# Performance work log

Hardware: AMD Instinct MI355X
Metric: run time of the kernel (lower is better)

The kernel has to match this reference:

```python
import jax, jax.numpy as jnp
import numpy as np

V, E, H, O, T = 50000, 300, 512, 64, 21
B, S = 256, 128


def setup_inputs() -> dict:
    key = jax.random.key(0)
    ks = jax.random.split(key, 20)
    u = lambda k, shape, s: jax.random.uniform(k, shape, jnp.float32, -s, s)
    sg = 1.0 / np.sqrt(H)
    s2 = 1.0 / np.sqrt(2 * H)
    return {
        "x": jax.random.randint(ks[0], (B, S), 0, V),
        "ner_tags": jax.random.randint(ks[1], (B, S), 0, T),
        "mask": jnp.ones((B, S), dtype=bool),
        "emb": jax.random.normal(ks[2], (V, E), jnp.float32) * 0.1,
        "W_ih_f": u(ks[3], (3 * H, E), sg),
        "W_hh_f": u(ks[4], (3 * H, H), sg),
        "b_ih_f": u(ks[5], (3 * H,), sg),
        "b_hh_f": u(ks[6], (3 * H,), sg),
        "W_ih_b": u(ks[7], (3 * H, E), sg),
        "W_hh_b": u(ks[8], (3 * H, H), sg),
        "b_ih_b": u(ks[9], (3 * H,), sg),
        "b_hh_b": u(ks[10], (3 * H,), sg),
        "attn_w": u(ks[11], (1, 2 * H), s2),
        "attn_b": u(ks[12], (1,), s2),
        "fc_w": u(ks[13], (O, 2 * H), s2),
        "fc_b": u(ks[14], (O,), s2),
        "ner_w": u(ks[15], (T, 2 * H), s2),
        "ner_b": u(ks[16], (T,), s2),
        "crf_start": u(ks[17], (T,), 0.1),
        "crf_end": u(ks[18], (T,), 0.1),
        "crf_trans": u(ks[19], (T, T), 0.1),
    }


def _gru_dir(xp, h0, W_hh, b_hh, reverse):
    # xp: [S, B, 3H] precomputed input projections (PyTorch GRU gate order r,z,n)
    def step(h, xpt):
        hp = h @ W_hh.T + b_hh
        xr, xz, xn = jnp.split(xpt, 3, axis=-1)
        hr, hz, hn = jnp.split(hp, 3, axis=-1)
        r = jax.nn.sigmoid(xr + hr)
        z = jax.nn.sigmoid(xz + hz)
        n = jnp.tanh(xn + r * hn)
        h_new = (1.0 - z) * n + z * h
        return h_new, h_new
    _, hs = jax.lax.scan(step, h0, xp, reverse=reverse)
    return hs  # [S, B, H]


def _crf_nll(emissions, tags, mask, start, end, trans):
    # emissions: [B, S, T]; torchcrf forward algorithm, reduction='mean'
    dt = emissions.dtype
    em_t = jnp.transpose(emissions, (1, 0, 2))        # [S, B, T]
    m_t = jnp.transpose(mask, (1, 0))                  # [S, B]

    def step(score, inp):
        em, m = inp
        # [B,T,1] + [1,T,T] + [B,1,T] -> logsumexp over prev tag
        ns = jax.nn.logsumexp(score[:, :, None] + trans[None] + em[:, None, :], axis=1)
        score = jnp.where(m[:, None], ns, score)
        return score, None

    score0 = start[None, :] + em_t[0]
    score, _ = jax.lax.scan(step, score0, (em_t[1:], m_t[1:]))
    logZ = jax.nn.logsumexp(score + end[None, :], axis=1)  # [B]

    mf = mask.astype(dt)
    em_sc = jnp.take_along_axis(emissions, tags[..., None], axis=2)[..., 0]  # [B,S]
    tr_sc = trans[tags[:, :-1], tags[:, 1:]]                                  # [B,S-1]
    seq_ends = jnp.sum(mask, axis=1).astype(jnp.int32) - 1
    last_tags = jnp.take_along_axis(tags, seq_ends[:, None].astype(tags.dtype), axis=1)[:, 0]
    num = (start[tags[:, 0]] + em_sc[:, 0]
           + jnp.sum((em_sc[:, 1:] + tr_sc) * mf[:, 1:], axis=1)
           + end[last_tags])
    return -jnp.mean(num - logZ)


def _forward(x, ner_tags, mask, emb,
             W_ih_f, W_hh_f, b_ih_f, b_hh_f,
             W_ih_b, W_hh_b, b_ih_b, b_hh_b,
             attn_w, attn_b, fc_w, fc_b, ner_w, ner_b,
             crf_start, crf_end, crf_trans):
    b = x.shape[0]
    xe = emb[x]                                  # [B,S,E]
    xs = jnp.transpose(xe, (1, 0, 2))            # [S,B,E]
    h0 = jnp.zeros((b, H), dtype=emb.dtype)
    xpf = jnp.einsum('sbe,ge->sbg', xs, W_ih_f) + b_ih_f
    hf = _gru_dir(xpf, h0, W_hh_f, b_hh_f, False)
    xpb = jnp.einsum('sbe,ge->sbg', xs, W_ih_b) + b_ih_b
    hb = _gru_dir(xpb, h0, W_hh_b, b_hh_b, True)
    gru_out = jnp.transpose(jnp.concatenate([hf, hb], axis=-1), (1, 0, 2))  # [B,S,2H]

    # attention pooling over seq dim (no masking, as in original)
    scores = gru_out @ attn_w.T + attn_b          # [B,S,1]
    w = jax.nn.softmax(scores, axis=1)
    ctx = jnp.sum(w * gru_out, axis=1)            # [B,2H]
    intent_logits = ctx @ fc_w.T + fc_b           # [B,O]  (dropout = identity in eval)

    emissions = gru_out @ ner_w.T + ner_b         # [B,S,T]
    ner_loss = _crf_nll(emissions, ner_tags, mask, crf_start, crf_end, crf_trans)
    return intent_logits, ner_loss


def reference(x, ner_tags, mask, emb,
              W_ih_f, W_hh_f, b_ih_f, b_hh_f,
              W_ih_b, W_hh_b, b_ih_b, b_hh_b,
              attn_w, attn_b, fc_w, fc_b, ner_w, ner_b,
              crf_start, crf_end, crf_trans):
    return _forward(x, ner_tags, mask, emb,
                    W_ih_f, W_hh_f, b_ih_f, b_hh_f,
                    W_ih_b, W_hh_b, b_ih_b, b_hh_b,
                    attn_w, attn_b, fc_w, fc_b, ner_w, ner_b,
                    crf_start, crf_end, crf_trans)
```

## Files before the change

### kernel.cpp

```cpp
#include <hip/hip_runtime.h>
#include <hip/hip_cooperative_groups.h>
#include <stdint.h>

namespace cg = cooperative_groups;

typedef __attribute__((ext_vector_type(8))) short s8_t;
typedef __attribute__((ext_vector_type(4))) short s4v_t;
typedef __attribute__((ext_vector_type(4))) float f4_t;
typedef unsigned short u16;

#define V_  50000
#define E_  300
#define EP_ 320
#define H_  512
#define G_  1536
#define O_  64
#define T_  21
#define B_  256
#define S_  128
#define BS_ 32768

__device__ __forceinline__ float b2f(u16 u) {
    union { unsigned int u; float f; } v; v.u = ((unsigned int)u) << 16; return v.f;
}
__device__ __forceinline__ u16 f2b(float f) {
    union { float f; unsigned int u; } v; v.f = f;
    unsigned int r = v.u + 0x7fffu + ((v.u >> 16) & 1u);
    return (u16)(r >> 16);
}
__device__ __forceinline__ float fsig(float x) {
    return __builtin_amdgcn_rcpf(1.f + __expf(-x));
}
__device__ __forceinline__ float ftanh(float x) {
    return 1.f - 2.f * __builtin_amdgcn_rcpf(1.f + __expf(2.f * x));
}

__global__ void prep_kernel(const float* wih_f, const float* wih_b,
                            const float* whh_f, const float* whh_b,
                            const float* ner_w,
                            u16* wih_bf, u16* whh_bf, u16* nerw_bf)
{
    const int NW = 3072 * EP_;
    const int NH = 2 * G_ * H_;
    const int NN = 32 * 1024;
    int stride = gridDim.x * blockDim.x;
    for (int i = blockIdx.x * blockDim.x + threadIdx.x; i < NW + NH + NN; i += stride) {
        if (i < NW) {
            int n = i / EP_, k = i % EP_;
            float v = 0.f;
            if (k < E_) v = (n < G_) ? wih_f[n * E_ + k] : wih_b[(n - G_) * E_ + k];
            wih_bf[i] = f2b(v);
        } else if (i < NW + NH) {
            int j = i - NW;
            int d = j / (G_ * H_), r = j % (G_ * H_);
            whh_bf[j] = f2b(d == 0 ? whh_f[r] : whh_b[r]);
        } else {
            int j = i - NW - NH;
            int t = j / 1024, k = j % 1024;
            nerw_bf[j] = f2b(t < T_ ? ner_w[t * 1024 + k] : 0.f);
        }
    }
}

__global__ void gather_kernel(const int* x, const float* emb, u16* xe)
{
    int stride = gridDim.x * blockDim.x;
    for (int i = blockIdx.x * blockDim.x + threadIdx.x; i < BS_ * EP_; i += stride) {
        int m = i / EP_, k = i % EP_;
        int s = m >> 8, b = m & 255;
        float v = 0.f;
        if (k < E_) v = emb[(size_t)x[b * S_ + s] * E_ + k];
        xe[i] = f2b(v);
    }
}

#define XST 328
__global__ __launch_bounds__(512, 2) void gru_persist(
    const u16* __restrict__ xe, const u16* __restrict__ wih,
    const float* bih_f, const float* bih_b,
    const u16* __restrict__ whh_bf,
    const float* bhh_f, const float* bhh_b,
    u16* h_hi, unsigned int* flag, unsigned int* xcnt)
{
    __shared__ u16 sWx[48 * XST];
    __shared__ f4_t red[4][4][64];
    __shared__ unsigned int role_sh[2];

    cg::grid_group grid = cg::this_grid();
    int tid = threadIdx.x, l = tid & 63, wid = tid >> 6;

    if (tid == 0) {
        unsigned int xcc = __builtin_amdgcn_s_getreg((7u << 11) | 20u) & 7u;
        unsigned int slot = __hip_atomic_fetch_add(&xcnt[xcc], 1u,
                                __ATOMIC_RELAXED, __HIP_MEMORY_SCOPE_AGENT);
        role_sh[0] = xcc; role_sh[1] = slot;
    }
    grid.sync();
    bool fast = true;
    for (int i = 0; i < 8; ++i)
        fast = fast && (__hip_atomic_load(&xcnt[i], __ATOMIC_RELAXED,
                            __HIP_MEMORY_SCOPE_AGENT) == 32u);
    int g, hs;
    if (fast) { g = (int)role_sh[0]; hs = (int)role_sh[1]; }
    else      { g = blockIdx.x >> 5; hs = blockIdx.x & 31; }
    int dir = g >> 2, bt = g & 3;
    int wpair = wid & 3;
    int khi   = wid >> 2;
    int r0  = bt * 64 + wpair * 16;
    int hc0 = hs * 16;
    int lr = l & 15, lk = (l >> 4) * 8;
    int koff_h = khi ? 256 : 0;
    int koff_x = khi ? 160 : 0;

    for (int idx = tid; idx < 48 * 40; idx += 512) {
        int rr = idx / 40, ck = (idx % 40) * 8;
        int gcol = (rr >> 4) * H_ + hc0 + (rr & 15);
        size_t goff = ((size_t)dir * G_ + gcol) * (size_t)EP_ + ck;
        *(s8_t*)&sWx[rr * XST + ck] = *(const s8_t*)&wih[goff];
    }

    s8_t Bh[3][8];
#pragma unroll
    for (int c = 0; c < 3; ++c)
#pragma unroll
        for (int kk = 0; kk < 8; ++kk)
            Bh[c][kk] = *(const s8_t*)&whh_bf[
                ((size_t)dir * G_ + c * H_ + hc0 + lr) * (size_t)H_ + koff_h + lk + kk * 32];
    __syncthreads();

    int lc = l & 15, lr4 = (l >> 4) * 4;
    int hc = hc0 + lc;
    const float* bih = dir ? bih_b : bih_f;
    const float* bhh = dir ? bhh_b : bhh_f;
    float br  = bih[hc] + bhh[hc];
    float bz  = bih[H_ + hc] + bhh[H_ + hc];
    float bxn = bih[2 * H_ + hc];
    float bhn = bhh[2 * H_ + hc];
    float hstate[4] = {0.f, 0.f, 0.f, 0.f};

    f4_t xac[3];
    auto xgemm = [&](int ttx) {
#pragma unroll
        for (int c = 0; c < 3; ++c) xac[c] = (f4_t){0.f, 0.f, 0.f, 0.f};
        const u16* xp = xe + ((size_t)ttx * B_ + r0 + lr) * EP_ + koff_x + lk;
#pragma unroll
        for (int kk = 0; kk < 5; ++kk) {
            s8_t ax = *(const s8_t*)(xp + kk * 32);
#pragma unroll
            for (int c = 0; c < 3; ++c) {
                s8_t bx = *(const s8_t*)&sWx[(c * 16 + lr) * XST + koff_x + lk + kk * 32];
                xac[c] = __builtin_amdgcn_mfma_f32_16x16x32_bf16(ax, bx, xac[c], 0, 0, 0);
            }
        }
    };

    xgemm(dir ? (S_ - 1) : 0);

#pragma unroll 1
    for (int t = 0; t < S_; ++t) {
        int tt = dir ? (S_ - 1 - t) : t;

        if (t > 0) {
            if (fast) {
                const unsigned int* fp = flag + g * 32 + khi * 16 + (l & 15);
                unsigned int tgt = (unsigned int)t;
                int spin = 0;
                for (;;) {
                    unsigned int v = tgt;
                    if (l < 16) v = __hip_atomic_load(fp, __ATOMIC_RELAXED,
                                                      __HIP_MEMORY_SCOPE_AGENT);
                    if (__all((int)(v >= tgt))) break;
                    if (++spin > 2) __builtin_amdgcn_s_sleep(1);
                }
                asm volatile("" ::: "memory");
            } else {
                __threadfence();
                grid.sync();
                __threadfence();
            }
        }

        f4_t ahn = {0.f, 0.f, 0.f, 0.f};
        if (t > 0) {
            int prev = dir ? (tt + 1) : (tt - 1);
            const u16* hb = h_hi + ((size_t)dir * S_ + prev) * B_ * H_
                                 + (size_t)(r0 + lr) * H_ + koff_h + lk;
            s8_t ah[8];
#pragma unroll
            for (int kk = 0; kk < 8; ++kk) ah[kk] = *(const s8_t*)(hb + kk * 32);
#pragma unroll
            for (int kk = 0; kk < 8; ++kk) {
                xac[0] = __builtin_amdgcn_mfma_f32_16x16x32_bf16(ah[kk], Bh[0][kk], xac[0], 0, 0, 0);
                xac[1] = __builtin_amdgcn_mfma_f32_16x16x32_bf16(ah[kk], Bh[1][kk], xac[1], 0, 0, 0);
                ahn    = __builtin_amdgcn_mfma_f32_16x16x32_bf16(ah[kk], Bh[2][kk], ahn,    0, 0, 0);
            }
        }

        if (khi) {
            red[0][wpair][l] = xac[0];
            red[1][wpair][l] = xac[1];
            red[2][wpair][l] = xac[2];
            red[3][wpair][l] = ahn;
        }
        __syncthreads();
        if (!khi) {
            f4_t q0 = red[0][wpair][l];
            f4_t q1 = red[1][wpair][l];
            f4_t q2 = red[2][wpair][l];
            f4_t q3 = red[3][wpair][l];
            u16* hw = h_hi + ((size_t)dir * S_ + tt) * B_ * H_;
#pragma unroll
            for (int r = 0; r < 4; ++r) {
                int row = r0 + lr4 + r;
                float pre_r = xac[0][r] + q0[r] + br;
                float pre_z = xac[1][r] + q1[r] + bz;
                float xn  = xac[2][r] + q2[r] + bxn;
                float hnv = ahn[r] + q3[r] + bhn;
                float rg = fsig(pre_r);
                float zg = fsig(pre_z);
                float ng = ftanh(xn + rg * hnv);
                float hnew = (1.f - zg) * ng + zg * hstate[r];
                hstate[r] = hnew;
                hw[(size_t)row * H_ + hc] = f2b(hnew);
            }
        }

        __syncthreads();
        if (t < S_ - 1) {
            if (fast && tid == 0)
                __hip_atomic_store(flag + g * 32 + hs, (unsigned int)(t + 1),
                                   __ATOMIC_RELAXED, __HIP_MEMORY_SCOPE_AGENT);
            xgemm(dir ? (S_ - 2 - t) : (t + 1));
        }
    }
}

__global__ __launch_bounds__(256) void scores_kernel(const u16* h_hi, const float* attn_w,
                                                     const float* attn_b, float* scores)
{
    int wid = threadIdx.x >> 6, l = threadIdx.x & 63;
    int row = blockIdx.x * 4 + wid;
    int dir = l >> 5;
    int hc = (l & 31) * 16;
    const u16* hp = h_hi + (size_t)dir * BS_ * H_ + (size_t)row * H_ + hc;
    s8_t v0 = *(const s8_t*)(hp);
    s8_t v1 = *(const s8_t*)(hp + 8);
    const float* aw = attn_w + dir * H_ + hc;
    float acc = 0.f;
#pragma unroll
    for (int j = 0; j < 8; ++j) acc += b2f((u16)v0[j]) * aw[j];
#pragma unroll
    for (int j = 0; j < 8; ++j) acc += b2f((u16)v1[j]) * aw[8 + j];
    for (int off = 32; off; off >>= 1) acc += __shfl_down(acc, off);
    if (l == 0) {
        int s = row >> 8, b = row & 255;
        scores[b * S_ + s] = acc + attn_b[0];
    }
}

__global__ __launch_bounds__(256) void attnctx_kernel(const u16* h_hi, const float* scores,
                                                      float* ctx)
{
    __shared__ float sc[S_];
    __shared__ float tmp[S_];
    int b = blockIdx.x, tid = threadIdx.x;
    if (tid < S_) sc[tid] = scores[b * S_ + tid];
    __syncthreads();
    if (tid < S_) tmp[tid] = sc[tid];
    __syncthreads();
    for (int st = 64; st > 0; st >>= 1) {
        if (tid < st) tmp[tid] = fmaxf(tmp[tid], tmp[tid + st]);
        __syncthreads();
    }
    float mx = tmp[0];
    __syncthreads();
    if (tid < S_) { sc[tid] = __expf(sc[tid] - mx); tmp[tid] = sc[tid]; }
    __syncthreads();
    for (int st = 64; st > 0; st >>= 1) {
        if (tid < st) tmp[tid] += tmp[tid + st];
        __syncthreads();
    }
    float inv = 1.f / tmp[0];
    __syncthreads();
    if (tid < S_) sc[tid] *= inv;
    __syncthreads();

    int c = tid * 4;
    int dir = c >> 9, hcv = c & (H_ - 1);
    const u16* hp = h_hi + (size_t)dir * BS_ * H_;
    float a0 = 0, a1 = 0, a2 = 0, a3 = 0;
    for (int s = 0; s < S_; ++s) {
        float w = sc[s];
        s4v_t v = *(const s4v_t*)(hp + ((size_t)s * B_ + b) * H_ + hcv);
        a0 += w * b2f((u16)v[0]); a1 += w * b2f((u16)v[1]);
        a2 += w * b2f((u16)v[2]); a3 += w * b2f((u16)v[3]);
    }
    float* cp = ctx + (size_t)b * 1024 + c;
    cp[0] = a0; cp[1] = a1; cp[2] = a2; cp[3] = a3;
}

__global__ __launch_bounds__(256) void intent_kernel(const float* ctx, const float* fc_w,
                                                     const float* fc_b, float* out)
{
    __shared__ float cs[1024];
    int b = blockIdx.x, tid = threadIdx.x;
    for (int i = tid; i < 1024; i += 256) cs[i] = ctx[(size_t)b * 1024 + i];
    __syncthreads();
    if (tid < O_) {
        float acc = fc_b[tid];
        const float* w = fc_w + (size_t)tid * 1024;
        for (int k = 0; k < 1024; ++k) acc += cs[k] * w[k];
        out[b * O_ + tid] = acc;
    }
}

__global__ __launch_bounds__(256) void emis_kernel(const u16* h_hi, const u16* nerw,
                                                   const float* ner_b, float* em)
{
    int tid = threadIdx.x, l = tid & 63, wid = tid >> 6;
    int rb = blockIdx.x * 64 + wid * 16;
    int lr = l & 15, lk = (l >> 4) * 8;
    f4_t acc[2] = {};
    for (int kk = 0; kk < 32; ++kk) {
        int k0 = kk * 32 + lk;
        int dir = k0 >> 9, hcv = k0 & (H_ - 1);
        s8_t a  = *(const s8_t*)(h_hi + (size_t)dir * BS_ * H_ + (size_t)(rb + lr) * H_ + hcv);
        s8_t b0 = *(const s8_t*)(nerw + (size_t)lr * 1024 + k0);
        s8_t b1 = *(const s8_t*)(nerw + (size_t)(16 + lr) * 1024 + k0);
        acc[0] = __builtin_amdgcn_mfma_f32_16x16x32_bf16(a, b0, acc[0], 0, 0, 0);
        acc[1] = __builtin_amdgcn_mfma_f32_16x16x32_bf16(a, b1, acc[1], 0, 0, 0);
    }
    int lc = l & 15, lr4 = (l >> 4) * 4;
#pragma unroll
    for (int f = 0; f < 2; ++f) {
        int tcol = f * 16 + lc;
        if (tcol < T_) {
            float nb = ner_b[tcol];
#pragma unroll
            for (int r = 0; r < 4; ++r) {
                int row = rb + lr4 + r;
                int s = row >> 8, bb = row & 255;
                em[((size_t)bb * S_ + s) * T_ + tcol] = acc[f][r] + nb;
            }
        }
    }
}

__global__ void num_kernel(const int* tags, const float* em, const float* cstart,
                           const float* cend, const float* ctrans, float* numv)
{
    int b = blockIdx.x * blockDim.x + threadIdx.x;
    if (b >= B_) return;
    const int* tg = tags + b * S_;
    int prev = tg[0];
    float acc = cstart[prev] + em[((size_t)b * S_) * T_ + prev];
    for (int s = 1; s < S_; ++s) {
        int tc = tg[s];
        acc += em[((size_t)b * S_ + s) * T_ + tc] + ctrans[prev * T_ + tc];
        prev = tc;
    }
    acc += cend[prev];
    numv[b] = acc;
}

__global__ __launch_bounds__(64) void crf2_kernel(const float* em, const float* cstart,
                                                  const float* cend, const float* ctrans,
                                                  float* logZ)
{
    int b = blockIdx.x, l = threadIdx.x;
    bool act = l < T_;
    float E[T_];
#pragma unroll
    for (int i = 0; i < T_; ++i) E[i] = act ? __expf(ctrans[i * T_ + l]) : 0.f;
    const float* eb = em + (size_t)b * S_ * T_;
    float sc = act ? (cstart[l] + eb[l]) : -1e30f;
#pragma unroll 1
    for (int s = 1; s < S_; ++s) {
        float emv = act ? eb[s * T_ + l] : 0.f;
        float m = sc;
#pragma unroll
        for (int off = 16; off; off >>= 1) m = fmaxf(m, __shfl_xor(m, off, 32));
        float e = act ? __expf(sc - m) : 0.f;
        float sum = 0.f;
#pragma unroll
        for (int i = 0; i < T_; ++i) sum += __shfl(e, i, 32) * E[i];
        sc = act ? (m + __logf(sum) + emv) : -1e30f;
    }
    float fin = act ? (sc + cend[l]) : -1e30f;
    float m = fin;
#pragma unroll
    for (int off = 16; off; off >>= 1) m = fmaxf(m, __shfl_xor(m, off, 32));
    float z = act ? __expf(fin - m) : 0.f;
#pragma unroll
    for (int off = 16; off; off >>= 1) z += __shfl_xor(z, off, 32);
    if (l == 0) logZ[b] = m + __logf(z);
}

__global__ __launch_bounds__(256) void loss_kernel(const float* numv, const float* logZ,
                                                   float* out)
{
    __shared__ float red[B_];
    int t = threadIdx.x;
    red[t] = numv[t] - logZ[t];
    __syncthreads();
    for (int st = 128; st > 0; st >>= 1) {
        if (t < st) red[t] += red[t + st];
        __syncthreads();
    }
    if (t == 0) out[16384] = -red[0] / (float)B_;
}

extern "C" void kernel_launch(void* const* d_in, const int* in_sizes, int n_in,
                              void* d_out, int out_size, void* d_ws, size_t ws_size,
                              hipStream_t stream)
{
    const int*   x      = (const int*)  d_in[0];
    const int*   tags   = (const int*)  d_in[1];
    const float* emb    = (const float*)d_in[3];
    const float* wih_f  = (const float*)d_in[4];
    const float* whh_f  = (const float*)d_in[5];
    const float* bih_f  = (const float*)d_in[6];
    const float* bhh_f  = (const float*)d_in[7];
    const float* wih_b  = (const float*)d_in[8];
    const float* whh_b  = (const float*)d_in[9];
    const float* bih_b  = (const float*)d_in[10];
    const float* bhh_b  = (const float*)d_in[11];
    const float* attn_w = (const float*)d_in[12];
    const float* attn_b = (const float*)d_in[13];
    const float* fc_w   = (const float*)d_in[14];
    const float* fc_b   = (const float*)d_in[15];
    const float* ner_w  = (const float*)d_in[16];
    const float* ner_b  = (const float*)d_in[17];
    const float* cstart = (const float*)d_in[18];
    const float* cend   = (const float*)d_in[19];
    const float* ctrans = (const float*)d_in[20];
    float* out = (float*)d_out;

    char* p = (char*)d_ws;
    auto alloc = [&](size_t bytes) { void* r = (void*)p; p += (bytes + 255) & ~(size_t)255; return r; };
    u16* wih_bf  = (u16*)alloc((size_t)3072 * EP_ * 2);
    u16* whh_bf  = (u16*)alloc((size_t)2 * G_ * H_ * 2);
    u16* nerw_bf = (u16*)alloc((size_t)32 * 1024 * 2);
    u16* xe      = (u16*)alloc((size_t)BS_ * EP_ * 2);
    u16* h_hi    = (u16*)alloc((size_t)2 * BS_ * H_ * 2);
    unsigned int* flag = (unsigned int*)alloc(8 * 32 * 4);
    unsigned int* xcnt = (unsigned int*)alloc(64);
    float* scores= (float*)alloc((size_t)BS_ * 4);
    float* ctx   = (float*)alloc((size_t)B_ * 1024 * 4);
    float* em    = (float*)alloc((size_t)B_ * S_ * T_ * 4);
    float* numv  = (float*)alloc(1024);
    float* logZ  = (float*)alloc(1024);

    hipMemsetAsync(flag, 0, 8 * 32 * 4, stream);
    hipMemsetAsync(xcnt, 0, 64, stream);

    hipLaunchKernelGGL(prep_kernel, dim3(2048), dim3(256), 0, stream,
                       wih_f, wih_b, whh_f, whh_b, ner_w, wih_bf, whh_bf, nerw_bf);
    hipLaunchKernelGGL(gather_kernel, dim3(4096), dim3(256), 0, stream, x, emb, xe);

    void* args[] = { &xe, &wih_bf, &bih_f, &bih_b, &whh_bf, &bhh_f, &bhh_b,
                     &h_hi, &flag, &xcnt };
    hipLaunchCooperativeKernel((const void*)gru_persist, dim3(256), dim3(512), args, 0, stream);

    hipLaunchKernelGGL(scores_kernel, dim3(BS_ / 4), dim3(256), 0, stream,
                       h_hi, attn_w, attn_b, scores);
    hipLaunchKernelGGL(attnctx_kernel, dim3(B_), dim3(256), 0, stream, h_hi, scores, ctx);
    hipLaunchKernelGGL(intent_kernel, dim3(B_), dim3(256), 0, stream, ctx, fc_w, fc_b, out);
    hipLaunchKernelGGL(emis_kernel, dim3(BS_ / 64), dim3(256), 0, stream, h_hi, nerw_bf, ner_b, em);
    hipLaunchKernelGGL(num_kernel, dim3(1), dim3(256), 0, stream, tags, em, cstart, cend, ctrans, numv);
    hipLaunchKernelGGL(crf2_kernel, dim3(B_), dim3(64), 0, stream, em, cstart, cend, ctrans, logZ);
    hipLaunchKernelGGL(loss_kernel, dim3(1), dim3(256), 0, stream, numv, logZ, out);
}
```

Measured before the change: 845.9 us.

## Split GRU persistent kernel into 512 smaller blocks and parallelize CRF numerator

The persistent GRU kernel now launches 512 blocks of 256 threads instead of 256 blocks of 512. Each block covers 32 batch rows instead of 64, with 8 batch tiles per direction and 64 blocks per XCD. The intent is to spread the recurrent matmul across more CUs and cut per-step latency, at the cost of more inter-block flag synchronization and duplicated weight loading per block. The CRF numerator kernel also moves from one thread per batch doing a serial loop to one wave per batch with a shuffle reduction.

```diff
diff --git a/kernel.cpp b/kernel.cpp
--- a/kernel.cpp
+++ b/kernel.cpp
@@ -75,7 +75,7 @@
 }
 
 #define XST 328
-__global__ __launch_bounds__(512, 2) void gru_persist(
+__global__ __launch_bounds__(256, 2) void gru_persist(
     const u16* __restrict__ xe, const u16* __restrict__ wih,
     const float* bih_f, const float* bih_b,
     const u16* __restrict__ whh_bf,
@@ -83,7 +83,7 @@
     u16* h_hi, unsigned int* flag, unsigned int* xcnt)
 {
     __shared__ u16 sWx[48 * XST];
-    __shared__ f4_t red[4][4][64];
+    __shared__ f4_t red[4][2][64];
     __shared__ unsigned int role_sh[2];
 
     cg::grid_group grid = cg::this_grid();
@@ -99,20 +99,25 @@
     bool fast = true;
     for (int i = 0; i < 8; ++i)
         fast = fast && (__hip_atomic_load(&xcnt[i], __ATOMIC_RELAXED,
-                            __HIP_MEMORY_SCOPE_AGENT) == 32u);
+                            __HIP_MEMORY_SCOPE_AGENT) == 64u);
     int g, hs;
-    if (fast) { g = (int)role_sh[0]; hs = (int)role_sh[1]; }
-    else      { g = blockIdx.x >> 5; hs = blockIdx.x & 31; }
-    int dir = g >> 2, bt = g & 3;
-    int wpair = wid & 3;
-    int khi   = wid >> 2;
-    int r0  = bt * 64 + wpair * 16;
+    if (fast) {
+        unsigned int xcc = role_sh[0], slot = role_sh[1];
+        g  = (int)(xcc * 2 + (slot >> 5));
+        hs = (int)(slot & 31);
+    } else {
+        g = blockIdx.x >> 5; hs = blockIdx.x & 31;
+    }
+    int dir = g >> 3, bt = g & 7;
+    int wpair = wid & 1;
+    int khi   = wid >> 1;
+    int r0  = bt * 32 + wpair * 16;
     int hc0 = hs * 16;
     int lr = l & 15, lk = (l >> 4) * 8;
     int koff_h = khi ? 256 : 0;
     int koff_x = khi ? 160 : 0;
 
-    for (int idx = tid; idx < 48 * 40; idx += 512) {
+    for (int idx = tid; idx < 48 * 40; idx += 256) {
         int rr = idx / 40, ck = (idx % 40) * 8;
         int gcol = (rr >> 4) * H_ + hc0 + (rr & 15);
         size_t goff = ((size_t)dir * G_ + gcol) * (size_t)EP_ + ck;
@@ -346,21 +351,23 @@
     }
 }
 
-__global__ void num_kernel(const int* tags, const float* em, const float* cstart,
-                           const float* cend, const float* ctrans, float* numv)
-{
-    int b = blockIdx.x * blockDim.x + threadIdx.x;
-    if (b >= B_) return;
+__global__ __launch_bounds__(64) void num_kernel(const int* tags, const float* em,
+                                                 const float* cstart, const float* cend,
+                                                 const float* ctrans, float* numv)
+{
+    int b = blockIdx.x, l = threadIdx.x;
     const int* tg = tags + b * S_;
-    int prev = tg[0];
-    float acc = cstart[prev] + em[((size_t)b * S_) * T_ + prev];
-    for (int s = 1; s < S_; ++s) {
+    float acc = 0.f;
+#pragma unroll
+    for (int q = 0; q < 2; ++q) {
+        int s = l + q * 64;
         int tc = tg[s];
-        acc += em[((size_t)b * S_ + s) * T_ + tc] + ctrans[prev * T_ + tc];
-        prev = tc;
-    }
-    acc += cend[prev];
-    numv[b] = acc;
+        acc += em[((size_t)b * S_ + s) * T_ + tc];
+        if (s > 0) acc += ctrans[tg[s - 1] * T_ + tc];
+    }
+#pragma unroll
+    for (int off = 32; off; off >>= 1) acc += __shfl_down(acc, off);
+    if (l == 0) numv[b] = acc + cstart[tg[0]] + cend[tg[S_ - 1]];
 }
 
 __global__ __launch_bounds__(64) void crf2_kernel(const float* em, const float* cstart,
@@ -443,7 +450,7 @@
     u16* nerw_bf = (u16*)alloc((size_t)32 * 1024 * 2);
     u16* xe      = (u16*)alloc((size_t)BS_ * EP_ * 2);
     u16* h_hi    = (u16*)alloc((size_t)2 * BS_ * H_ * 2);
-    unsigned int* flag = (unsigned int*)alloc(8 * 32 * 4);
+    unsigned int* flag = (unsigned int*)alloc(16 * 32 * 4);
     unsigned int* xcnt = (unsigned int*)alloc(64);
     float* scores= (float*)alloc((size_t)BS_ * 4);
     float* ctx   = (float*)alloc((size_t)B_ * 1024 * 4);
@@ -451,7 +458,7 @@
     float* numv  = (float*)alloc(1024);
     float* logZ  = (float*)alloc(1024);
 
-    hipMemsetAsync(flag, 0, 8 * 32 * 4, stream);
+    hipMemsetAsync(flag, 0, 16 * 32 * 4, stream);
     hipMemsetAsync(xcnt, 0, 64, stream);
 
     hipLaunchKernelGGL(prep_kernel, dim3(2048), dim3(256), 0, stream,
@@ -460,14 +467,14 @@
 
     void* args[] = { &xe, &wih_bf, &bih_f, &bih_b, &whh_bf, &bhh_f, &bhh_b,
                      &h_hi, &flag, &xcnt };
-    hipLaunchCooperativeKernel((const void*)gru_persist, dim3(256), dim3(512), args, 0, stream);
+    hipLaunchCooperativeKernel((const void*)gru_persist, dim3(512), dim3(256), args, 0, stream);
 
     hipLaunchKernelGGL(scores_kernel, dim3(BS_ / 4), dim3(256), 0, stream,
                        h_hi, attn_w, attn_b, scores);
     hipLaunchKernelGGL(attnctx_kernel, dim3(B_), dim3(256), 0, stream, h_hi, scores, ctx);
     hipLaunchKernelGGL(intent_kernel, dim3(B_), dim3(256), 0, stream, ctx, fc_w, fc_b, out);
     hipLaunchKernelGGL(emis_kernel, dim3(BS_ / 64), dim3(256), 0, stream, h_hi, nerw_bf, ner_b, em);
-    hipLaunchKernelGGL(num_kernel, dim3(1), dim3(256), 0, stream, tags, em, cstart, cend, ctrans, numv);
+    hipLaunchKernelGGL(num_kernel, dim3(B_), dim3(64), 0, stream, tags, em, cstart, cend, ctrans, numv);
     hipLaunchKernelGGL(crf2_kernel, dim3(B_), dim3(64), 0, stream, em, cstart, cend, ctrans, logZ);
     hipLaunchKernelGGL(loss_kernel, dim3(1), dim3(256), 0, stream, numv, logZ, out);
 }
```

New measurement: 808.2 us. -4.5%, faster.
